# Optimization experiments

Hardware: AMD Instinct MI355X
Metric: run time of the kernel (lower is better)

## Reference

```python
import jax, jax.numpy as jnp
import numpy as np

EPS = 1e-5
A_BIT = 4
W_BIT = 4


def ste_round(x):
    # straight-through estimator round, matching torch quantize_fn
    return x + jax.lax.stop_gradient(jnp.round(x) - x)


def qk(x, k):
    n = float(2 ** k - 1)
    return ste_round(x * n) / n


def quant_w(w, k):
    # DoReFa weight quantization (Conv2d_Q_)
    t = jnp.tanh(w)
    t = t / (2.0 * jnp.max(jnp.abs(t))) + 0.5
    return 2.0 * qk(t, k) - 1.0


def act_q(x, k):
    # Activate: ReLU then clamp to [0,1] then k-bit quantize
    return qk(jnp.clip(jax.nn.relu(x), 0.0, 1.0), k)


def bn(x, g, b, m, v):
    # inference-mode BatchNorm2d / SwitchBatchNorm2d over NCHW
    scale = (g * jax.lax.rsqrt(v + EPS))[None, :, None, None]
    shift = b[None, :, None, None] - m[None, :, None, None] * scale
    return x * scale + shift


def conv(x, w, stride, pad):
    return jax.lax.conv_general_dilated(
        x, w, (stride, stride), ((pad, pad), (pad, pad)),
        dimension_numbers=('NCHW', 'OIHW', 'NCHW'))


def setup_inputs() -> dict:
    key = jax.random.key(0)
    ks = jax.random.split(key, 16)
    N, Cin, Cout, H = 256, 64, 128, 32
    return {
        'x':  jax.random.normal(ks[0], (N, Cin, H, H), jnp.float32),
        'w1': jax.random.normal(ks[1], (Cout, Cin, 3, 3), jnp.float32),
        'w2': jax.random.normal(ks[2], (Cout, Cout, 3, 3), jnp.float32),
        'ws': jax.random.normal(ks[3], (Cout, Cin, 1, 1), jnp.float32),
        'g1': jax.random.uniform(ks[4], (Cin,), jnp.float32),
        'b1': jax.random.normal(ks[5], (Cin,), jnp.float32),
        'm1': jax.random.normal(ks[6], (Cin,), jnp.float32),
        'v1': jax.random.uniform(ks[7], (Cin,), jnp.float32),
        'g2': jax.random.uniform(ks[8], (Cout,), jnp.float32),
        'b2': jax.random.normal(ks[9], (Cout,), jnp.float32),
        'm2': jax.random.normal(ks[10], (Cout,), jnp.float32),
        'v2': jax.random.uniform(ks[11], (Cout,), jnp.float32),
        'gs': jax.random.uniform(ks[12], (Cin,), jnp.float32),
        'bs': jax.random.normal(ks[13], (Cin,), jnp.float32),
        'ms': jax.random.normal(ks[14], (Cin,), jnp.float32),
        'vs': jax.random.uniform(ks[15], (Cin,), jnp.float32),
    }


def reference(x, w1, w2, ws, g1, b1, m1, v1, g2, b2, m2, v2, gs, bs, ms, vs):
    # out = conv1(act1(bn1(x)))  (dropout is identity in eval)
    out = conv(act_q(bn(x, g1, b1, m1, v1), A_BIT), quant_w(w1, W_BIT), 2, 1)
    # out = conv2(act2(bn2(out)))
    out = conv(act_q(bn(out, g2, b2, m2, v2), A_BIT), quant_w(w2, W_BIT), 1, 1)
    # shortcut: plain BN -> 1x1 conv, stride 2
    sc = conv(bn(x, gs, bs, ms, vs), ws, 2, 0)
    return out + sc
```

## Files before the change

kernel.cpp:

```cpp
#include <hip/hip_runtime.h>
#include <hip/hip_bf16.h>


typedef __bf16 bf16x8 __attribute__((ext_vector_type(8)));
typedef float f32x4 __attribute__((ext_vector_type(4)));
typedef int i32x4 __attribute__((ext_vector_type(4)));

#define EPSV 1e-5f

__global__ __launch_bounds__(256) void k_wmax(const float* __restrict__ w1,
                                              const float* __restrict__ w2,
                                              float* __restrict__ wpart) {
    int sel = blockIdx.x >> 4;
    const float* src = sel ? w2 : w1;
    int cnt = sel ? 128 * 128 * 9 : 128 * 64 * 9;
    float m = 0.f;
    for (int i = (blockIdx.x & 15) * 256 + threadIdx.x; i < cnt; i += 16 * 256)
        m = fmaxf(m, fabsf(src[i]));
#pragma unroll
    for (int off = 32; off > 0; off >>= 1)
        m = fmaxf(m, __shfl_down(m, off));
    __shared__ float red[4];
    if ((threadIdx.x & 63) == 0) red[threadIdx.x >> 6] = m;
    __syncthreads();
    if (threadIdx.x == 0)
        wpart[blockIdx.x] = fmaxf(fmaxf(red[0], red[1]), fmaxf(red[2], red[3]));
}

__global__ void k_bnprep(const float* g1, const float* b1, const float* m1, const float* v1,
                         const float* g2, const float* b2, const float* m2, const float* v2,
                         const float* gs, const float* bs, const float* ms, const float* vs,
                         const float* __restrict__ wpart, float* bnp) {
    int c = threadIdx.x;
    if (c < 64) {
        float s = g1[c] * rsqrtf(v1[c] + EPSV);
        bnp[c] = s;          bnp[64 + c] = b1[c] - m1[c] * s;
        float s2 = gs[c] * rsqrtf(vs[c] + EPSV);
        bnp[128 + c] = s2;   bnp[192 + c] = bs[c] - ms[c] * s2;
    }
    float s = g2[c] * rsqrtf(v2[c] + EPSV);
    bnp[256 + c] = s;        bnp[384 + c] = b2[c] - m2[c] * s;
    if (c < 2) {
        float m = 0.f;
#pragma unroll
        for (int i = 0; i < 16; ++i) m = fmaxf(m, wpart[c * 16 + i]);
        bnp[512 + c] = 15.f / (2.f * tanhf(m));
    }
}

__global__ __launch_bounds__(256) void k_wq_all(
        const float* __restrict__ w1, const float* __restrict__ w2,
        const float* __restrict__ wsw,
        signed char* __restrict__ w1qi, signed char* __restrict__ w2qi,
        __bf16* __restrict__ wsq, const float* __restrict__ bnp) {
    int b = blockIdx.x, t = threadIdx.x;
    if (b < 864) {
        bool isw1 = b < 288;
        int idx = (isw1 ? b : b - 288) * 256 + t;
        float c = bnp[512 + (isw1 ? 0 : 1)];
        int kk = idx & 63;
        int co = (idx >> 6) & 127;
        int s = idx >> 13;
        int k = s * 64 + kk;
        int khw, ci;
        const float* src;
        if (isw1) { khw = k >> 6; ci = k & 63;  src = w1 + (co * 64 + ci) * 9 + khw; }
        else      { khw = k >> 7; ci = k & 127; src = w2 + (co * 128 + ci) * 9 + khw; }
        int j = (int)rintf(tanhf(*src) * c + 7.5f);
        (isw1 ? w1qi : w2qi)[idx] = (signed char)(2 * j - 15);
    } else {
        int idx = (b - 864) * 256 + t;
        int kk = idx & 31;
        int co = (idx >> 5) & 127;
        int s = idx >> 12;
        wsq[idx] = (__bf16)wsw[co * 64 + s * 32 + kk];
    }
}

__global__ __launch_bounds__(1024, 4) void k_mega(
        const float* __restrict__ x,
        const signed char* __restrict__ w1qi,
        const signed char* __restrict__ w2qi,
        const __bf16* __restrict__ wsq,
        const float* __restrict__ bnp,
        float* __restrict__ out) {
    __shared__ __align__(16) char lds_all[73984 + 41472 + 32768];
    signed char* slab = (signed char*)lds_all;
    signed char* a2p  = (signed char*)(lds_all + 73984);
    char*        ascb = lds_all + 73984 + 41472;

    const int t = threadIdx.x;
    const int n = blockIdx.x;
    const int wv = t >> 6, l = t & 63;
    const int lrow = l & 15, quad = l >> 4;

    if (t < 528) {
        int ci_ = t >> 2, sub = t & 3;
        int cell;
        if (ci_ < 34)      cell = ci_;
        else if (ci_ < 68) cell = 33 * 34 + (ci_ - 34);
        else { int k = ci_ - 68; cell = (1 + (k >> 1)) * 34 + (k & 1) * 33; }
        *(uint4*)(slab + cell * 64 + sub * 16) = uint4{0u, 0u, 0u, 0u};
    }
    if (t < 544) {
        int ci_ = t >> 3, sub = t & 7;
        int cell;
        if (ci_ < 18)      cell = ci_;
        else if (ci_ < 36) cell = 17 * 18 + (ci_ - 18);
        else { int k = ci_ - 36; cell = (1 + (k >> 1)) * 18 + (k & 1) * 17; }
        *(uint4*)(a2p + cell * 128 + sub * 16) = uint4{0u, 0u, 0u, 0u};
    }

#pragma unroll
    for (int it = 0; it < 4; ++it) {
        int u = t + it * 1024;
        int wq = u & 255;
        int cq = u >> 8;
        int p0 = wq * 4;
        int h = p0 >> 5, w0 = p0 & 31;
        int c0 = cq * 4;
        float4 s1 = *(const float4*)(bnp + c0);
        float4 h1 = *(const float4*)(bnp + 64 + c0);
        float4 ssv = *(const float4*)(bnp + 128 + c0);
        float4 hsv = *(const float4*)(bnp + 192 + c0);
        const float* s1p = (const float*)&s1;
        const float* h1p = (const float*)&h1;
        const float* ssp = (const float*)&ssv;
        const float* hsp = (const float*)&hsv;
        f32x4 xr[4];
#pragma unroll
        for (int j = 0; j < 4; ++j)
            xr[j] = __builtin_nontemporal_load(
                (const f32x4*)(x + ((size_t)(n * 64 + c0 + j)) * 1024 + p0));
#pragma unroll
        for (int k = 0; k < 4; ++k) {
            unsigned u32 = 0;
#pragma unroll
            for (int j = 0; j < 4; ++j) {
                float xv = xr[j][k];
                float v = xv * s1p[j] + h1p[j];
                int q = (int)rintf(fminf(fmaxf(v, 0.f), 1.f) * 15.f);
                u32 |= (unsigned)q << (8 * j);
            }
            int pw = w0 + k + 1, ph = h + 1;
            int cell = ph * 34 + pw;
            int key = (pw >> 1) & 3;
            *(unsigned*)(slab + cell * 64 + (((cq >> 2) ^ key) * 16) + (cq & 3) * 4) = u32;
        }
        if ((h & 1) == 0) {
#pragma unroll
            for (int k = 0; k < 4; k += 2) {
                int w = w0 + k;
                __bf16 bv[4];
#pragma unroll
                for (int j = 0; j < 4; ++j) {
                    float xv = xr[j][k];
                    bv[j] = (__bf16)(xv * ssp[j] + hsp[j]);
                }
                int cell = (h >> 1) * 16 + (w >> 1);
                int key = (w >> 1) & 7;
                *(uint2*)(ascb + cell * 128 + (((cq >> 1) ^ key) * 16) + (cq & 1) * 8) =
                    *(uint2*)bv;
            }
        }
    }
    __syncthreads();

    const int wco = wv & 1;
    const int wpos = wv >> 1;

    {
        i32x4 acc1[4][2] = {};
#pragma unroll
        for (int s = 0; s < 9; ++s) {
            const int kh = s / 3, kw = s % 3;
            i32x4 af[4];
#pragma unroll
            for (int i = 0; i < 4; ++i)
                af[i] = *(const i32x4*)(w1qi +
                    ((s * 128 + wco * 64 + i * 16 + lrow) * 64 + quad * 16));
            i32x4 bf[2];
#pragma unroll
            for (int j = 0; j < 2; ++j) {
                int h2 = wpos * 2 + j;
                int ph = 2 * h2 + kh;
                int pw = 2 * lrow + kw;
                int key = (pw >> 1) & 3;
                bf[j] = *(const i32x4*)(slab + (ph * 34 + pw) * 64 + ((quad ^ key) * 16));
            }
#pragma unroll
            for (int i = 0; i < 4; ++i)
#pragma unroll
                for (int j = 0; j < 2; ++j)
                    acc1[i][j] = __builtin_amdgcn_mfma_i32_16x16x64_i8(af[i], bf[j], acc1[i][j], 0, 0, 0);
        }
#pragma unroll
        for (int i = 0; i < 4; ++i) {
            const int co0 = wco * 64 + i * 16 + quad * 4;
            float4 s2 = *(const float4*)(bnp + 256 + co0);
            float4 h2f = *(const float4*)(bnp + 384 + co0);
            const float* s2p = (const float*)&s2;
            const float* h2p = (const float*)&h2f;
#pragma unroll
            for (int j = 0; j < 2; ++j) {
                int h2 = wpos * 2 + j, w2 = lrow;
                unsigned u32 = 0;
#pragma unroll
                for (int r = 0; r < 4; ++r) {
                    float v = (float)acc1[i][j][r] * (s2p[r] * (1.f / 225.f)) + h2p[r];
                    int q = (int)rintf(fminf(fmaxf(v, 0.f), 1.f) * 15.f);
                    u32 |= (unsigned)q << (8 * r);
                }
                int cell = (h2 + 1) * 18 + (w2 + 1);
                int key = (w2 + 1) & 7;
                *(unsigned*)(a2p + cell * 128 + ((((co0 >> 4) ^ key)) * 16) + (co0 & 15)) = u32;
            }
        }
    }
    __syncthreads();

    {
        i32x4 acc2[4][2] = {};
#pragma unroll
        for (int s = 0; s < 18; ++s) {
            const int khw = s >> 1, cis = s & 1;
            const int kh = khw / 3, kw = khw % 3;
            i32x4 af[4];
#pragma unroll
            for (int i = 0; i < 4; ++i)
                af[i] = *(const i32x4*)(w2qi +
                    ((s * 128 + wco * 64 + i * 16 + lrow) * 64 + quad * 16));
            i32x4 bf[2];
#pragma unroll
            for (int j = 0; j < 2; ++j) {
                int h2 = wpos * 2 + j;
                int ph = h2 + kh, pw = lrow + kw;
                int chunk = cis * 4 + quad;
                int key = pw & 7;
                bf[j] = *(const i32x4*)(a2p + (ph * 18 + pw) * 128 + ((chunk ^ key) * 16));
            }
#pragma unroll
            for (int i = 0; i < 4; ++i)
#pragma unroll
                for (int j = 0; j < 2; ++j)
                    acc2[i][j] = __builtin_amdgcn_mfma_i32_16x16x64_i8(af[i], bf[j], acc2[i][j], 0, 0, 0);
        }
        f32x4 accM[4][2];
#pragma unroll
        for (int i = 0; i < 4; ++i)
#pragma unroll
            for (int j = 0; j < 2; ++j)
#pragma unroll
                for (int r = 0; r < 4; ++r)
                    accM[i][j][r] = (float)acc2[i][j][r] * (1.f / 225.f);
#pragma unroll
        for (int s = 0; s < 2; ++s) {
            bf16x8 af[4], bb[2];
#pragma unroll
            for (int i = 0; i < 4; ++i)
                af[i] = *(const bf16x8*)(wsq + (size_t)s * 4096 +
                    ((wco * 64 + i * 16 + lrow) * 32 + quad * 8));
#pragma unroll
            for (int j = 0; j < 2; ++j) {
                int h2 = wpos * 2 + j, w2 = lrow;
                int cell = h2 * 16 + w2;
                int sub = s * 4 + quad;
                bb[j] = *(const bf16x8*)(ascb + cell * 128 + ((sub ^ (w2 & 7)) * 16));
            }
#pragma unroll
            for (int i = 0; i < 4; ++i)
#pragma unroll
                for (int j = 0; j < 2; ++j)
                    accM[i][j] = __builtin_amdgcn_mfma_f32_16x16x32_bf16(af[i], bb[j], accM[i][j], 0, 0, 0);
        }
#pragma unroll
        for (int i = 0; i < 4; ++i) {
            const int co0 = wco * 64 + i * 16 + quad * 4;
#pragma unroll
            for (int j = 0; j < 2; ++j) {
                int pos = (wpos * 2 + j) * 16 + lrow;
#pragma unroll
                for (int r = 0; r < 4; ++r)
                    __builtin_nontemporal_store(accM[i][j][r],
                        out + ((size_t)n * 128 + co0 + r) * 256 + pos);
            }
        }
    }
}

extern "C" void kernel_launch(void* const* d_in, const int* in_sizes, int n_in,
                              void* d_out, int out_size, void* d_ws, size_t ws_size,
                              hipStream_t stream) {
    const float* x   = (const float*)d_in[0];
    const float* w1  = (const float*)d_in[1];
    const float* w2  = (const float*)d_in[2];
    const float* wsw = (const float*)d_in[3];
    const float* g1  = (const float*)d_in[4];
    const float* b1  = (const float*)d_in[5];
    const float* m1  = (const float*)d_in[6];
    const float* v1  = (const float*)d_in[7];
    const float* g2  = (const float*)d_in[8];
    const float* b2  = (const float*)d_in[9];
    const float* m2  = (const float*)d_in[10];
    const float* v2  = (const float*)d_in[11];
    const float* gs  = (const float*)d_in[12];
    const float* bs  = (const float*)d_in[13];
    const float* ms  = (const float*)d_in[14];
    const float* vs  = (const float*)d_in[15];
    float* out = (float*)d_out;
    char* ws = (char*)d_ws;

    signed char* w1qi = (signed char*)(ws);
    signed char* w2qi = (signed char*)(ws + 73728);
    __bf16*      wsq  = (__bf16*)(ws + 221184);
    float*       bnp  = (float*)(ws + 237568);
    float*       wprt = (float*)(ws + 240128);

    k_wmax<<<32, 256, 0, stream>>>(w1, w2, wprt);
    k_bnprep<<<1, 128, 0, stream>>>(g1, b1, m1, v1, g2, b2, m2, v2,
                                    gs, bs, ms, vs, wprt, bnp);
    k_wq_all<<<896, 256, 0, stream>>>(w1, w2, wsw, w1qi, w2qi, wsq, bnp);
    k_mega<<<256, 1024, 0, stream>>>(x, w1qi, w2qi, wsq, bnp, out);
}
```

Before: 57.92 us.

## Stage conv weights through LDS in chunks and compute shortcut first

```diff
diff --git a/kernel.cpp b/kernel.cpp
--- a/kernel.cpp
+++ b/kernel.cpp
@@ -93,6 +93,8 @@
     const int n = blockIdx.x;
     const int wv = t >> 6, l = t & 63;
     const int lrow = l & 15, quad = l >> 4;
+    const int wco = wv & 1;
+    const int wpos = wv >> 1;
 
     if (t < 528) {
         int ci_ = t >> 2, sub = t & 3;
@@ -166,33 +168,64 @@
     }
     __syncthreads();
 
-    const int wco = wv & 1;
-    const int wpos = wv >> 1;
+    f32x4 accF[4][2] = {};
+#pragma unroll
+    for (int s = 0; s < 2; ++s) {
+        bf16x8 af[4], bb[2];
+#pragma unroll
+        for (int i = 0; i < 4; ++i)
+            af[i] = *(const bf16x8*)(wsq + (size_t)s * 4096 +
+                ((wco * 64 + i * 16 + lrow) * 32 + quad * 8));
+#pragma unroll
+        for (int j = 0; j < 2; ++j) {
+            int cell = (wpos * 2 + j) * 16 + lrow;
+            int sub = s * 4 + quad;
+            bb[j] = *(const bf16x8*)(ascb + cell * 128 + ((sub ^ (lrow & 7)) * 16));
+        }
+#pragma unroll
+        for (int i = 0; i < 4; ++i)
+#pragma unroll
+            for (int j = 0; j < 2; ++j)
+                accF[i][j] = __builtin_amdgcn_mfma_f32_16x16x32_bf16(af[i], bb[j], accF[i][j], 0, 0, 0);
+    }
+    __syncthreads();
 
     {
+        char* wlds2 = ascb;
         i32x4 acc1[4][2] = {};
-#pragma unroll
-        for (int s = 0; s < 9; ++s) {
-            const int kh = s / 3, kw = s % 3;
-            i32x4 af[4];
-#pragma unroll
-            for (int i = 0; i < 4; ++i)
-                af[i] = *(const i32x4*)(w1qi +
-                    ((s * 128 + wco * 64 + i * 16 + lrow) * 64 + quad * 16));
-            i32x4 bf[2];
-#pragma unroll
-            for (int j = 0; j < 2; ++j) {
-                int h2 = wpos * 2 + j;
-                int ph = 2 * h2 + kh;
-                int pw = 2 * lrow + kw;
-                int key = (pw >> 1) & 3;
-                bf[j] = *(const i32x4*)(slab + (ph * 34 + pw) * 64 + ((quad ^ key) * 16));
-            }
-#pragma unroll
-            for (int i = 0; i < 4; ++i)
-#pragma unroll
-                for (int j = 0; j < 2; ++j)
-                    acc1[i][j] = __builtin_amdgcn_mfma_i32_16x16x64_i8(af[i], bf[j], acc1[i][j], 0, 0, 0);
+#pragma unroll 1
+        for (int chunk = 0; chunk < 3; ++chunk) {
+            const int s0 = chunk * 4;
+            const int ns = (chunk == 2) ? 1 : 4;
+            for (int c = t; c < ns * 512; c += 1024)
+                *(uint4*)(wlds2 + c * 16) =
+                    *(const uint4*)(w1qi + (size_t)s0 * 8192 + c * 16);
+            __syncthreads();
+#pragma unroll 1
+            for (int sl = 0; sl < ns; ++sl) {
+                const int s = s0 + sl;
+                const int kh = (s * 11) >> 5, kw = s - 3 * kh;
+                i32x4 af[4];
+#pragma unroll
+                for (int i = 0; i < 4; ++i)
+                    af[i] = *(const i32x4*)(wlds2 +
+                        ((sl * 128 + wco * 64 + i * 16 + lrow) * 64 + quad * 16));
+                i32x4 bf[2];
+#pragma unroll
+                for (int j = 0; j < 2; ++j) {
+                    int h2 = wpos * 2 + j;
+                    int ph = 2 * h2 + kh;
+                    int pw = 2 * lrow + kw;
+                    int key = (pw >> 1) & 3;
+                    bf[j] = *(const i32x4*)(slab + (ph * 34 + pw) * 64 + ((quad ^ key) * 16));
+                }
+#pragma unroll
+                for (int i = 0; i < 4; ++i)
+#pragma unroll
+                    for (int j = 0; j < 2; ++j)
+                        acc1[i][j] = __builtin_amdgcn_mfma_i32_16x16x64_i8(af[i], bf[j], acc1[i][j], 0, 0, 0);
+            }
+            __syncthreads();
         }
 #pragma unroll
         for (int i = 0; i < 4; ++i) {
@@ -217,61 +250,42 @@
             }
         }
     }
-    __syncthreads();
 
     {
+        char* wlds3 = (char*)slab;
         i32x4 acc2[4][2] = {};
-#pragma unroll
-        for (int s = 0; s < 18; ++s) {
-            const int khw = s >> 1, cis = s & 1;
-            const int kh = khw / 3, kw = khw % 3;
-            i32x4 af[4];
-#pragma unroll
-            for (int i = 0; i < 4; ++i)
-                af[i] = *(const i32x4*)(w2qi +
-                    ((s * 128 + wco * 64 + i * 16 + lrow) * 64 + quad * 16));
-            i32x4 bf[2];
-#pragma unroll
-            for (int j = 0; j < 2; ++j) {
-                int h2 = wpos * 2 + j;
-                int ph = h2 + kh, pw = lrow + kw;
-                int chunk = cis * 4 + quad;
-                int key = pw & 7;
-                bf[j] = *(const i32x4*)(a2p + (ph * 18 + pw) * 128 + ((chunk ^ key) * 16));
-            }
-#pragma unroll
-            for (int i = 0; i < 4; ++i)
-#pragma unroll
-                for (int j = 0; j < 2; ++j)
-                    acc2[i][j] = __builtin_amdgcn_mfma_i32_16x16x64_i8(af[i], bf[j], acc2[i][j], 0, 0, 0);
-        }
-        f32x4 accM[4][2];
-#pragma unroll
-        for (int i = 0; i < 4; ++i)
-#pragma unroll
-            for (int j = 0; j < 2; ++j)
-#pragma unroll
-                for (int r = 0; r < 4; ++r)
-                    accM[i][j][r] = (float)acc2[i][j][r] * (1.f / 225.f);
-#pragma unroll
-        for (int s = 0; s < 2; ++s) {
-            bf16x8 af[4], bb[2];
-#pragma unroll
-            for (int i = 0; i < 4; ++i)
-                af[i] = *(const bf16x8*)(wsq + (size_t)s * 4096 +
-                    ((wco * 64 + i * 16 + lrow) * 32 + quad * 8));
-#pragma unroll
-            for (int j = 0; j < 2; ++j) {
-                int h2 = wpos * 2 + j, w2 = lrow;
-                int cell = h2 * 16 + w2;
-                int sub = s * 4 + quad;
-                bb[j] = *(const bf16x8*)(ascb + cell * 128 + ((sub ^ (w2 & 7)) * 16));
-            }
-#pragma unroll
-            for (int i = 0; i < 4; ++i)
-#pragma unroll
-                for (int j = 0; j < 2; ++j)
-                    accM[i][j] = __builtin_amdgcn_mfma_f32_16x16x32_bf16(af[i], bb[j], accM[i][j], 0, 0, 0);
+#pragma unroll 1
+        for (int half = 0; half < 2; ++half) {
+            const signed char* src = w2qi + (size_t)half * 73728;
+            for (int c = t; c < 4608; c += 1024)
+                *(uint4*)(wlds3 + c * 16) = *(const uint4*)(src + c * 16);
+            __syncthreads();
+#pragma unroll 1
+            for (int sl = 0; sl < 9; ++sl) {
+                const int s = half * 9 + sl;
+                const int khw = s >> 1, cis = s & 1;
+                const int kh = (khw * 11) >> 5, kw = khw - 3 * kh;
+                i32x4 af[4];
+#pragma unroll
+                for (int i = 0; i < 4; ++i)
+                    af[i] = *(const i32x4*)(wlds3 +
+                        ((sl * 128 + wco * 64 + i * 16 + lrow) * 64 + quad * 16));
+                i32x4 bf[2];
+#pragma unroll
+                for (int j = 0; j < 2; ++j) {
+                    int h2 = wpos * 2 + j;
+                    int ph = h2 + kh, pw = lrow + kw;
+                    int chunkk = cis * 4 + quad;
+                    int key = pw & 7;
+                    bf[j] = *(const i32x4*)(a2p + (ph * 18 + pw) * 128 + ((chunkk ^ key) * 16));
+                }
+#pragma unroll
+                for (int i = 0; i < 4; ++i)
+#pragma unroll
+                    for (int j = 0; j < 2; ++j)
+                        acc2[i][j] = __builtin_amdgcn_mfma_i32_16x16x64_i8(af[i], bf[j], acc2[i][j], 0, 0, 0);
+            }
+            __syncthreads();
         }
 #pragma unroll
         for (int i = 0; i < 4; ++i) {
@@ -280,9 +294,11 @@
             for (int j = 0; j < 2; ++j) {
                 int pos = (wpos * 2 + j) * 16 + lrow;
 #pragma unroll
-                for (int r = 0; r < 4; ++r)
-                    __builtin_nontemporal_store(accM[i][j][r],
+                for (int r = 0; r < 4; ++r) {
+                    float v = (float)acc2[i][j][r] * (1.f / 225.f) + accF[i][j][r];
+                    __builtin_nontemporal_store(v,
                         out + ((size_t)n * 128 + co0 + r) * 256 + pos);
+                }
             }
         }
     }
```

Result: faster. 48.56 us (-16.2%).
